# Kernel tuning notes

Measured on AMD Instinct MI355X. Metric: run time of the kernel, lower is better.

The kernel has to match this reference:

```python
import jax, jax.numpy as jnp
import numpy as np
from math import sqrt

HEADS = 16
D_MODEL = 1024
HEAD_DIM = D_MODEL // HEADS  # 64
B, SEQ = 2, 2048


def setup_inputs() -> dict:
    key = jax.random.key(0)
    ks = jax.random.split(key, 8)
    k = jax.random.normal(ks[0], (B, SEQ, D_MODEL), dtype=jnp.float32)
    q = jax.random.normal(ks[1], (B, SEQ, D_MODEL), dtype=jnp.float32)
    v = jax.random.normal(ks[2], (B, SEQ, D_MODEL), dtype=jnp.float32)
    # causal mask, broadcast over batch and heads; masked_fill where mask == 0
    mask = jnp.tril(jnp.ones((SEQ, SEQ), dtype=jnp.int32))[None, None, :, :]
    s = 1.0 / sqrt(HEAD_DIM)
    Wq = jax.random.normal(ks[3], (HEAD_DIM, HEAD_DIM), dtype=jnp.float32) * s
    Wk = jax.random.normal(ks[4], (HEAD_DIM, HEAD_DIM), dtype=jnp.float32) * s
    Wv = jax.random.normal(ks[5], (HEAD_DIM, HEAD_DIM), dtype=jnp.float32) * s
    Wo = jax.random.normal(ks[6], (D_MODEL, D_MODEL), dtype=jnp.float32) * (1.0 / sqrt(D_MODEL))
    bo = jax.random.normal(ks[7], (D_MODEL,), dtype=jnp.float32) * 0.01
    return {"key": k, "query": q, "value": v, "mask": mask,
            "Wq": Wq, "Wk": Wk, "Wv": Wv, "Wo": Wo, "bo": bo}


def reference(key, query, value, mask, Wq, Wk, Wv, Wo, bo):
    b, q_len, d = query.shape
    k_len = key.shape[1]
    hd = d // HEADS
    # reshape to [b, len, heads, head_dim]
    k = key.reshape(b, k_len, HEADS, hd)
    q = query.reshape(b, q_len, HEADS, hd)
    v = value.reshape(b, k_len, HEADS, hd)
    # per-head-dim Linear (weights shared across heads); torch Linear: y = x @ W.T
    k = jnp.einsum('bkhd,ed->bkhe', k, Wk)
    q = jnp.einsum('bqhd,ed->bqhe', q, Wq)
    v = jnp.einsum('bvhd,ed->bvhe', v, Wv)
    # full attention matrix [b, h, q, k]
    product = jnp.einsum('bqhd,bkhd->bhqk', q, k)
    # NOTE: original masks BEFORE scaling by 1/sqrt(head_dim)
    product = jnp.where(mask == 0, jnp.float32(-1e20), product)
    product = product / jnp.float32(sqrt(hd))
    score = jax.nn.softmax(product, axis=-1)
    out = jnp.einsum('bhqv,bvhd->bqhd', score, v).reshape(b, q_len, d)
    out = out @ Wo.T + bo
    return out
```

## Files before the change

### kernel.cpp

```cpp
#include <hip/hip_runtime.h>

typedef __bf16 bf16x8 __attribute__((ext_vector_type(8)));
typedef float  f32x4  __attribute__((ext_vector_type(4)));
typedef unsigned int uint32x4 __attribute__((ext_vector_type(4)));

#define MFMA16(a, b, c) __builtin_amdgcn_mfma_f32_16x16x32_bf16((a), (b), (c), 0, 0, 0)

constexpr int SEQ = 2048;
constexpr int DM  = 1024;
constexpr int NH  = 16;
constexpr int HD  = 64;
constexpr int BATCH = 2;


__device__ inline bf16x8 ld8_f32(const float* p) {
    f32x4 a = *(const f32x4*)p;
    f32x4 b = *(const f32x4*)(p + 4);
    bf16x8 r;
    r[0] = (__bf16)a[0]; r[1] = (__bf16)a[1]; r[2] = (__bf16)a[2]; r[3] = (__bf16)a[3];
    r[4] = (__bf16)b[0]; r[5] = (__bf16)b[1]; r[6] = (__bf16)b[2]; r[7] = (__bf16)b[3];
    return r;
}

__global__ __launch_bounds__(256)
void proj_kernel(const float* __restrict__ Xq, const float* __restrict__ Xk,
                 const float* __restrict__ Xv,
                 const float* __restrict__ Wq, const float* __restrict__ Wk,
                 const float* __restrict__ Wv,
                 __bf16* __restrict__ Qp, __bf16* __restrict__ Kp,
                 __bf16* __restrict__ Vp)
{
    const int tid  = threadIdx.x;
    const int w    = tid >> 6;
    const int lane = tid & 63;
    const int quad = lane >> 4;
    const int l16  = lane & 15;
    const int sblk = blockIdx.x;
    const int bh   = blockIdx.y;
    const int tz   = blockIdx.z;

    const float* X = (tz == 0) ? Xq : (tz == 1) ? Xk : Xv;
    const float* W = (tz == 0) ? Wq : (tz == 1) ? Wk : Wv;
    __bf16*      O = (tz == 0) ? Qp : (tz == 1) ? Kp : Vp;
    const float scale = (tz == 0) ? (0.125f * 1.44269504088896f) : 1.0f;

    const int b = bh >> 4, h = bh & 15;
    const int mrow = sblk * 64 + w * 16 + l16;

    const size_t xoff = (size_t)(b * SEQ + mrow) * DM + h * HD + quad * 8;
    bf16x8 a0 = ld8_f32(X + xoff);
    bf16x8 a1 = ld8_f32(X + xoff + 32);

    f32x4 acc[4];
    #pragma unroll
    for (int nt = 0; nt < 4; ++nt) {
        const size_t woff = (size_t)(nt * 16 + l16) * HD + quad * 8;
        bf16x8 b0 = ld8_f32(W + woff);
        bf16x8 b1 = ld8_f32(W + woff + 32);
        f32x4 c = {0.f, 0.f, 0.f, 0.f};
        c = MFMA16(a0, b0, c);
        c = MFMA16(a1, b1, c);
        acc[nt] = c;
    }

    __bf16* obase = O + (size_t)bh * SEQ * HD;
    #pragma unroll
    for (int nt = 0; nt < 4; ++nt) {
        #pragma unroll
        for (int r = 0; r < 4; ++r) {
            const int srow = sblk * 64 + w * 16 + quad * 4 + r;
            obase[(size_t)srow * HD + nt * 16 + l16] = (__bf16)(acc[nt][r] * scale);
        }
    }
}

__global__ __launch_bounds__(256, 2)
void attn_kernel(const __bf16* __restrict__ Qp, const __bf16* __restrict__ Kp,
                 const __bf16* __restrict__ Vp, __bf16* __restrict__ AO)
{
    __shared__ __align__(16) unsigned int K_lds[2][64 * 36];
    __shared__ __align__(16) unsigned int VT2[2][64 * 36];
    __shared__ __align__(16) __bf16 P_lds[4][16 * 72];

    const int tid  = threadIdx.x;
    const int w    = tid >> 6;
    const int lane = tid & 63;
    const int quad = lane >> 4;
    const int l16  = lane & 15;
    const int pr   = blockIdx.x;
    const int bh   = blockIdx.y;

    const __bf16* Qb = Qp + (size_t)bh * SEQ * HD;
    const __bf16* Kb = Kp + (size_t)bh * SEQ * HD;
    const __bf16* Vb = Vp + (size_t)bh * SEQ * HD;

    bf16x8 onesf;
    #pragma unroll
    for (int i = 0; i < 8; ++i) onesf[i] = (l16 == 0) ? (__bf16)1.0f : (__bf16)0.0f;

    const int krow = tid >> 3, kcol = tid & 7;
    const int jp = tid & 31, d0 = (tid >> 5) * 8;

    #pragma unroll
    for (int phase = 0; phase < 2; ++phase) {
        const int tile = (phase == 0) ? (31 - pr) : pr;
        const int q0   = tile * 64;
        const int nkc  = tile + 1;

        __syncthreads();

        const int mrow = q0 + w * 16 + l16;
        bf16x8 qa0 = *(const bf16x8*)(Qb + (size_t)mrow * HD + quad * 8);
        bf16x8 qa1 = *(const bf16x8*)(Qb + (size_t)mrow * HD + quad * 8 + 32);

        f32x4 accO[4];
        #pragma unroll
        for (int nt = 0; nt < 4; ++nt) { f32x4 z = {0.f,0.f,0.f,0.f}; accO[nt] = z; }
        f32x4 acc5 = {0.f, 0.f, 0.f, 0.f};

        uint32x4 kpre0 = *(const uint32x4*)(Kb + (size_t)krow * HD + kcol * 8);
        uint32x4 kpre1 = *(const uint32x4*)(Kb + (size_t)(krow + 32) * HD + kcol * 8);
        uint32x4 vlo   = *(const uint32x4*)(Vb + (size_t)(2 * jp) * HD + d0);
        uint32x4 vhi   = *(const uint32x4*)(Vb + (size_t)(2 * jp + 1) * HD + d0);

        for (int kc = 0; kc < nkc; ++kc) {
            const int buf = kc & 1;
            *(uint32x4*)&K_lds[buf][krow * 36 + kcol * 4]        = kpre0;
            *(uint32x4*)&K_lds[buf][(krow + 32) * 36 + kcol * 4] = kpre1;
            #pragma unroll
            for (int i2 = 0; i2 < 4; ++i2) {
                const unsigned int va = vlo[i2], vb = vhi[i2];
                VT2[buf][(d0 + 2 * i2    ) * 36 + jp] = (va & 0xffffu) | (vb << 16);
                VT2[buf][(d0 + 2 * i2 + 1) * 36 + jp] = (va >> 16) | (vb & 0xffff0000u);
            }
            __syncthreads();

            if (kc + 1 < nkc) {
                const size_t o = (size_t)(kc + 1) * 64;
                kpre0 = *(const uint32x4*)(Kb + (o + krow) * HD + kcol * 8);
                kpre1 = *(const uint32x4*)(Kb + (o + krow + 32) * HD + kcol * 8);
                vlo   = *(const uint32x4*)(Vb + (o + 2 * jp) * HD + d0);
                vhi   = *(const uint32x4*)(Vb + (o + 2 * jp + 1) * HD + d0);
            }

            f32x4 s[4];
            #pragma unroll
            for (int nt = 0; nt < 4; ++nt) {
                const unsigned int* kb = &K_lds[buf][(nt * 16 + l16) * 36 + quad * 4];
                bf16x8 kb0 = *(const bf16x8*)(kb);
                bf16x8 kb1 = *(const bf16x8*)(kb + 16);
                f32x4 c = {0.f, 0.f, 0.f, 0.f};
                c = MFMA16(qa0, kb0, c);
                c = MFMA16(qa1, kb1, c);
                s[nt] = c;
            }
            if (kc == tile) {
                #pragma unroll
                for (int nt = 0; nt < 4; ++nt) {
                    const int j = kc * 64 + nt * 16 + l16;
                    #pragma unroll
                    for (int r = 0; r < 4; ++r) {
                        const int qrow = q0 + w * 16 + quad * 4 + r;
                        if (j > qrow) s[nt][r] = -1e30f;
                    }
                }
            }
            #pragma unroll
            for (int nt = 0; nt < 4; ++nt) {
                #pragma unroll
                for (int r = 0; r < 4; ++r) {
                    P_lds[w][(quad * 4 + r) * 72 + nt * 16 + l16] =
                        (__bf16)exp2f(s[nt][r]);
                }
            }
            asm volatile("" ::: "memory");
            bf16x8 pa0 = *(const bf16x8*)&P_lds[w][l16 * 72 + quad * 8];
            bf16x8 pa1 = *(const bf16x8*)&P_lds[w][l16 * 72 + quad * 8 + 32];
            #pragma unroll
            for (int nt = 0; nt < 4; ++nt) {
                const unsigned int* vb2 = &VT2[buf][(nt * 16 + l16) * 36 + quad * 4];
                bf16x8 vb0 = *(const bf16x8*)(vb2);
                bf16x8 vb1 = *(const bf16x8*)(vb2 + 16);
                accO[nt] = MFMA16(pa0, vb0, accO[nt]);
                accO[nt] = MFMA16(pa1, vb1, accO[nt]);
            }
            acc5 = MFMA16(pa0, onesf, acc5);
            acc5 = MFMA16(pa1, onesf, acc5);
        }

        const int b = bh >> 4, h = bh & 15;
        float inv[4];
        #pragma unroll
        for (int r = 0; r < 4; ++r) {
            const float ls = __shfl(acc5[r], quad * 16, 64);
            inv[r] = 1.0f / ls;
        }
        #pragma unroll
        for (int nt = 0; nt < 4; ++nt) {
            #pragma unroll
            for (int r = 0; r < 4; ++r) {
                const int qrow = q0 + w * 16 + quad * 4 + r;
                AO[(size_t)(b * SEQ + qrow) * DM + h * HD + nt * 16 + l16] =
                    (__bf16)(accO[nt][r] * inv[r]);
            }
        }
    }
}

__global__ __launch_bounds__(256)
void ogemm_kernel(const __bf16* __restrict__ AO, const float* __restrict__ Wo,
                  const float* __restrict__ bo, float* __restrict__ out)
{
    __shared__ __align__(16) unsigned int A_lds[64 * 36];
    __shared__ __align__(16) unsigned int B_lds[128 * 36];

    const int tid  = threadIdx.x;
    const int w    = tid >> 6;
    const int lane = tid & 63;
    const int quad = lane >> 4;
    const int l16  = lane & 15;
    const int m0   = blockIdx.x * 64;
    const int n0   = blockIdx.y * 128;

    f32x4 acc[8];
    #pragma unroll
    for (int nt = 0; nt < 8; ++nt) { f32x4 z = {0.f,0.f,0.f,0.f}; acc[nt] = z; }

    for (int kc = 0; kc < DM / 64; ++kc) {
        __syncthreads();
        #pragma unroll
        for (int i = 0; i < 2; ++i) {
            const int id = tid + i * 256;
            const int row = id >> 3, c = id & 7;
            *(uint32x4*)&A_lds[row * 36 + c * 4] =
                *(const uint32x4*)(AO + (size_t)(m0 + row) * DM + kc * 64 + c * 8);
        }
        #pragma unroll
        for (int i = 0; i < 4; ++i) {
            const int id = tid + i * 256;
            const int row = id >> 3, c = id & 7;
            bf16x8 v = ld8_f32(Wo + (size_t)(n0 + row) * DM + kc * 64 + c * 8);
            *(uint32x4*)&B_lds[row * 36 + c * 4] = *(const uint32x4*)&v;
        }
        __syncthreads();
        #pragma unroll
        for (int ks = 0; ks < 2; ++ks) {
            bf16x8 a = *(const bf16x8*)&A_lds[(w * 16 + l16) * 36 + ks * 16 + quad * 4];
            #pragma unroll
            for (int nt = 0; nt < 8; ++nt) {
                bf16x8 bb = *(const bf16x8*)&B_lds[(nt * 16 + l16) * 36 + ks * 16 + quad * 4];
                acc[nt] = MFMA16(a, bb, acc[nt]);
            }
        }
    }

    #pragma unroll
    for (int nt = 0; nt < 8; ++nt) {
        const int n = n0 + nt * 16 + l16;
        const float bof = bo[n];
        #pragma unroll
        for (int r = 0; r < 4; ++r) {
            const int m = m0 + w * 16 + quad * 4 + r;
            out[(size_t)m * DM + n] = acc[nt][r] + bof;
        }
    }
}

extern "C" void kernel_launch(void* const* d_in, const int* in_sizes, int n_in,
                              void* d_out, int out_size, void* d_ws, size_t ws_size,
                              hipStream_t stream)
{
    const float* key   = (const float*)d_in[0];
    const float* query = (const float*)d_in[1];
    const float* value = (const float*)d_in[2];
    const float* Wq = (const float*)d_in[4];
    const float* Wk = (const float*)d_in[5];
    const float* Wv = (const float*)d_in[6];
    const float* Wo = (const float*)d_in[7];
    const float* bo = (const float*)d_in[8];

    const size_t per = (size_t)BATCH * NH * SEQ * HD;
    __bf16* Qp = (__bf16*)d_ws;
    __bf16* Kp = Qp + per;
    __bf16* Vp = Kp + per;
    __bf16* AO = Vp + per;

    proj_kernel<<<dim3(SEQ / 64, BATCH * NH, 3), 256, 0, stream>>>(
        query, key, value, Wq, Wk, Wv, Qp, Kp, Vp);
    attn_kernel<<<dim3(SEQ / 128, BATCH * NH), 256, 0, stream>>>(Qp, Kp, Vp, AO);
    ogemm_kernel<<<dim3(BATCH * SEQ / 64, DM / 128), 256, 0, stream>>>(
        AO, Wo, bo, (float*)d_out);
}
```

Baseline: 223.9 us.

## Pre-convert Wo to bf16 and double-buffer output GEMM tiles with register prefetch

Adds a small kernel that converts Wo to bf16 once into reused workspace, so the output GEMM no longer reloads and converts fp32 weights in every block. The GEMM now prefetches the next K-chunk into registers while computing the current one, using double-buffered LDS with a single barrier per iteration. This adds a kernel launch and extra register pressure, and depends on Kp being dead after attention.

```diff
diff --git a/kernel.cpp b/kernel.cpp
--- a/kernel.cpp
+++ b/kernel.cpp
@@ -208,11 +208,18 @@
 }
 
 __global__ __launch_bounds__(256)
-void ogemm_kernel(const __bf16* __restrict__ AO, const float* __restrict__ Wo,
+void wconv_kernel(const float* __restrict__ Wo, __bf16* __restrict__ Wb)
+{
+    const size_t i = ((size_t)blockIdx.x * 256 + threadIdx.x) * 8;
+    *(bf16x8*)(Wb + i) = ld8_f32(Wo + i);
+}
+
+__global__ __launch_bounds__(256)
+void ogemm_kernel(const __bf16* __restrict__ AO, const __bf16* __restrict__ Wb,
                   const float* __restrict__ bo, float* __restrict__ out)
 {
-    __shared__ __align__(16) unsigned int A_lds[64 * 36];
-    __shared__ __align__(16) unsigned int B_lds[128 * 36];
+    __shared__ __align__(16) unsigned int A_lds[2][64 * 36];
+    __shared__ __align__(16) unsigned int B_lds[2][128 * 36];
 
     const int tid  = threadIdx.x;
     const int w    = tid >> 6;
@@ -222,33 +229,46 @@
     const int m0   = blockIdx.x * 64;
     const int n0   = blockIdx.y * 128;
 
+    const int row = tid >> 3, c = tid & 7;
+
     f32x4 acc[8];
     #pragma unroll
     for (int nt = 0; nt < 8; ++nt) { f32x4 z = {0.f,0.f,0.f,0.f}; acc[nt] = z; }
 
+    uint32x4 apre[2], bpre[4];
+    #pragma unroll
+    for (int i = 0; i < 2; ++i)
+        apre[i] = *(const uint32x4*)(AO + (size_t)(m0 + row + i * 32) * DM + c * 8);
+    #pragma unroll
+    for (int i = 0; i < 4; ++i)
+        bpre[i] = *(const uint32x4*)(Wb + (size_t)(n0 + row + i * 32) * DM + c * 8);
+
     for (int kc = 0; kc < DM / 64; ++kc) {
+        const int buf = kc & 1;
+        #pragma unroll
+        for (int i = 0; i < 2; ++i)
+            *(uint32x4*)&A_lds[buf][(row + i * 32) * 36 + c * 4] = apre[i];
+        #pragma unroll
+        for (int i = 0; i < 4; ++i)
+            *(uint32x4*)&B_lds[buf][(row + i * 32) * 36 + c * 4] = bpre[i];
         __syncthreads();
-        #pragma unroll
-        for (int i = 0; i < 2; ++i) {
-            const int id = tid + i * 256;
-            const int row = id >> 3, c = id & 7;
-            *(uint32x4*)&A_lds[row * 36 + c * 4] =
-                *(const uint32x4*)(AO + (size_t)(m0 + row) * DM + kc * 64 + c * 8);
-        }
-        #pragma unroll
-        for (int i = 0; i < 4; ++i) {
-            const int id = tid + i * 256;
-            const int row = id >> 3, c = id & 7;
-            bf16x8 v = ld8_f32(Wo + (size_t)(n0 + row) * DM + kc * 64 + c * 8);
-            *(uint32x4*)&B_lds[row * 36 + c * 4] = *(const uint32x4*)&v;
-        }
-        __syncthreads();
+
+        if (kc + 1 < DM / 64) {
+            const size_t o = (size_t)(kc + 1) * 64;
+            #pragma unroll
+            for (int i = 0; i < 2; ++i)
+                apre[i] = *(const uint32x4*)(AO + (size_t)(m0 + row + i * 32) * DM + o + c * 8);
+            #pragma unroll
+            for (int i = 0; i < 4; ++i)
+                bpre[i] = *(const uint32x4*)(Wb + (size_t)(n0 + row + i * 32) * DM + o + c * 8);
+        }
+
         #pragma unroll
         for (int ks = 0; ks < 2; ++ks) {
-            bf16x8 a = *(const bf16x8*)&A_lds[(w * 16 + l16) * 36 + ks * 16 + quad * 4];
+            bf16x8 a = *(const bf16x8*)&A_lds[buf][(w * 16 + l16) * 36 + ks * 16 + quad * 4];
             #pragma unroll
             for (int nt = 0; nt < 8; ++nt) {
-                bf16x8 bb = *(const bf16x8*)&B_lds[(nt * 16 + l16) * 36 + ks * 16 + quad * 4];
+                bf16x8 bb = *(const bf16x8*)&B_lds[buf][(nt * 16 + l16) * 36 + ks * 16 + quad * 4];
                 acc[nt] = MFMA16(a, bb, acc[nt]);
             }
         }
@@ -284,10 +304,12 @@
     __bf16* Kp = Qp + per;
     __bf16* Vp = Kp + per;
     __bf16* AO = Vp + per;
+    __bf16* Wb = Kp;
 
     proj_kernel<<<dim3(SEQ / 64, BATCH * NH, 3), 256, 0, stream>>>(
         query, key, value, Wq, Wk, Wv, Qp, Kp, Vp);
     attn_kernel<<<dim3(SEQ / 128, BATCH * NH), 256, 0, stream>>>(Qp, Kp, Vp, AO);
+    wconv_kernel<<<dim3(DM * DM / (256 * 8)), 256, 0, stream>>>(Wo, Wb);
     ogemm_kernel<<<dim3(BATCH * SEQ / 64, DM / 128), 256, 0, stream>>>(
-        AO, Wo, bo, (float*)d_out);
-}
+        AO, Wb, bo, (float*)d_out);
+}
```

Measured after the change: 198.7 us. -11.3%, faster.
